# Performance work log

Measured on AMD Instinct MI355X. Metric: run time of the kernel, lower is better.

Reference implementation:

```python
import jax, jax.numpy as jnp
import numpy as np

H = 256
EPS = 1e-5

def setup_inputs() -> dict:
    key = jax.random.key(0)
    ks = jax.random.split(key, 9)
    B, T = 2048, 512
    x = jax.random.randint(ks[0], (B, T, 1), 0, 10).astype(jnp.float32)
    # parameters (torch nn.Linear stores weight as [out,in]; we store [in,out])
    W_embed = jax.random.normal(ks[1], (1, H), jnp.float32) * 0.5
    b_embed = jax.random.normal(ks[2], (H,), jnp.float32) * 0.05
    W_update = jax.random.normal(ks[3], (H, H), jnp.float32) * (1.0 / np.sqrt(H))
    b_update = jax.random.normal(ks[4], (H,), jnp.float32) * 0.05
    gamma = jnp.ones((H,), jnp.float32)
    beta = jnp.zeros((H,), jnp.float32)
    W_out = jax.random.normal(ks[5], (H, 10), jnp.float32) * (1.0 / np.sqrt(H))
    b_out = jax.random.normal(ks[6], (10,), jnp.float32) * 0.05
    return {"x": x, "W_embed": W_embed, "b_embed": b_embed,
            "W_update": W_update, "b_update": b_update,
            "gamma": gamma, "beta": beta, "W_out": W_out, "b_out": b_out}

def _layernorm(h, gamma, beta):
    mu = jnp.mean(h, axis=-1, keepdims=True)
    var = jnp.mean(jnp.square(h - mu), axis=-1, keepdims=True)
    return (h - mu) * jax.lax.rsqrt(var + EPS) * gamma + beta

def reference(x, W_embed, b_embed, W_update, b_update, gamma, beta, W_out, b_out):
    B, T, _ = x.shape
    xt = jnp.transpose(x, (1, 0, 2))  # [T, B, 1]

    def step(h, x_t):
        inp = jnp.tanh(x_t @ W_embed + b_embed)           # [B, H]
        h = jnp.tanh((inp + h) @ W_update + b_update)     # [B, H]
        h = _layernorm(h, gamma, beta)
        return h, None

    h0 = jnp.zeros((B, H), x.dtype)
    h_final, _ = jax.lax.scan(step, h0, xt)
    return h_final @ W_out + b_out                        # [B, 10]
```

## Files before the change

### kernel.cpp

```cpp
#include <hip/hip_runtime.h>
#include <hip/hip_fp16.h>
#include <cstdint>

#define T_STEPS 512
#define HDIM    256
#define ROWS    8
#define LN_EPS  1e-5f

typedef _Float16 half8   __attribute__((ext_vector_type(8)));
typedef _Float16 half4v  __attribute__((ext_vector_type(4)));
typedef float    float4v __attribute__((ext_vector_type(4)));
typedef float    float2v __attribute__((ext_vector_type(2)));
typedef int      int4v   __attribute__((ext_vector_type(4)));
typedef int      int2v   __attribute__((ext_vector_type(2)));

#if __has_builtin(__builtin_amdgcn_permlane32_swap)
#define HAS_PL32 1
#else
#define HAS_PL32 0
#endif
#if __has_builtin(__builtin_amdgcn_permlane16_swap)
#define HAS_PL16 1
#else
#define HAS_PL16 0
#endif

struct __align__(16) Smem {
  _Float16 Bp[2][4096];
  float    gb[10][268];
  float    wg[260];
  float    wb[260];
  float    red[2][8][20];
  int      xi[8][516];
};

__device__ __forceinline__ float tanh_fast(float x) {
  float e = __expf(2.0f * x);
  float r = __builtin_amdgcn_rcpf(e + 1.0f);
  return fmaf(-2.0f, r, 1.0f);
}
__device__ __forceinline__ float dpp_ror8(float v) {
  return __int_as_float(__builtin_amdgcn_mov_dpp(__float_as_int(v), 0x128, 0xf, 0xf, true));
}
__device__ __forceinline__ float swz_xor16(float v) {
  return __int_as_float(__builtin_amdgcn_ds_swizzle(__float_as_int(v), 0x401F));
}
__device__ __forceinline__ float sum_xor16(float v) {
#if HAS_PL16
  int2v r2 = __builtin_amdgcn_permlane16_swap(__float_as_int(v), __float_as_int(v), false, false);
  return __int_as_float(r2[0]) + __int_as_float(r2[1]);
#else
  return v + swz_xor16(v);
#endif
}
__device__ __forceinline__ float sum_xor32(float v) {
#if HAS_PL32
  int2v r2 = __builtin_amdgcn_permlane32_swap(__float_as_int(v), __float_as_int(v), false, false);
  return __int_as_float(r2[0]) + __int_as_float(r2[1]);
#else
  return v + __shfl_xor(v, 32, 64);
#endif
}

__global__ __launch_bounds__(512, 1)
void rnn_scan_kernel(const float* __restrict__ x,
                     const float* __restrict__ we,  const float* __restrict__ be,
                     const float* __restrict__ Wu,  const float* __restrict__ bu,
                     const float* __restrict__ gma, const float* __restrict__ bta,
                     const float* __restrict__ Wo,  const float* __restrict__ bo,
                     float* __restrict__ out)
{
  __shared__ Smem sm;
  const int tid = threadIdx.x;
  const int wv  = tid >> 6;
  const int l   = tid & 63;
  const int q   = l >> 4;
  const int m   = l & 15;
  const int sel = m >> 3;
  const int r   = m & 7;
  const int r0  = blockIdx.x * ROWS;

  for (int i = tid; i < ROWS * T_STEPS; i += 512) {
    const int rr = i >> 9, c = i & (T_STEPS - 1);
    int xv = (int)x[(size_t)(r0 + rr) * T_STEPS + c];
    xv = xv < 0 ? 0 : (xv > 9 ? 9 : xv);
    sm.xi[rr][c] = xv;
  }
  if (tid < ROWS) {
    sm.xi[tid][512] = 0; sm.xi[tid][513] = 0;
    sm.xi[tid][514] = 0; sm.xi[tid][515] = 0;
  }

  float* et = reinterpret_cast<float*>(&sm.Bp[0][0]);
  if (tid < HDIM) {
    const float wek = we[tid], bek = be[tid];
    #pragma unroll
    for (int v = 0; v < 10; ++v)
      et[v*HDIM + tid] = tanh_fast(fmaf((float)v, wek, bek));
  }
  __syncthreads();

  {
    const int g = tid >> 8;
    const int n = tid & 255;
    float acc[5] = {0,0,0,0,0};
    float accx = 0.0f;
    const int vb = g * 5;
    for (int k = 0; k < HDIM; ++k) {
      const float wk = Wu[(size_t)k*HDIM + n];
      #pragma unroll
      for (int v = 0; v < 5; ++v) acc[v] = fmaf(et[(vb+v)*HDIM + k], wk, acc[v]);
      const float xk = g ? bta[k] : gma[k];
      accx = fmaf(xk, wk, accx);
    }
    const float bun = bu[n];
    #pragma unroll
    for (int v = 0; v < 5; ++v) sm.gb[vb+v][n] = acc[v] + bun;
    if (g == 0) sm.wg[n] = accx; else sm.wb[n] = accx;
  }
  __syncthreads();

  if (tid < HDIM) {
    const float wbn = sm.wb[tid];
    #pragma unroll
    for (int v = 0; v < 10; ++v) sm.gb[v][tid] += wbn;
  }
  {
    uint32_t* p = reinterpret_cast<uint32_t*>(&sm.Bp[0][0]);
    for (int i = tid; i < 4096; i += 512) p[i] = 0u;
  }
  if (tid < 320) (&sm.red[0][0][0])[tid] = 0.0f;

  half8 Whi[2][8], Wlo[2][8];
  #pragma unroll
  for (int nt = 0; nt < 2; ++nt) {
    const int n = wv*32 + nt*16 + m;
    #pragma unroll
    for (int kt = 0; kt < 8; ++kt) {
      const int k0 = kt*32 + q*8;
      half8 hi, lo;
      #pragma unroll
      for (int j = 0; j < 8; ++j) {
        float v = Wu[(size_t)(k0 + j)*HDIM + n];
        _Float16 h = (_Float16)v;
        hi[j] = h;
        lo[j] = (_Float16)((v - (float)h) * 2048.0f);
      }
      Whi[nt][kt] = hi; Wlo[nt][kt] = lo;
    }
  }
  const int n_sel = wv*32 + sel*16 + q*4;
  const float4v gmr = *reinterpret_cast<const float4v*>(&gma[n_sel]);
  __syncthreads();
  const float4v wgr = *reinterpret_cast<const float4v*>(&sm.wg[n_sel]);

  const float c1 = 4.8828125e-4f;
  const float* gbp = &sm.gb[0][n_sel];
  float4v th4;

  const int rdoff = l * 8;
  const int woff  = wv*512 + (2*sel + (q>>1))*128 + r*8 + (q&1)*4;

  int4v xQ = *reinterpret_cast<const int4v*>(&sm.xi[r][0]);
  float4v gbv_n = *reinterpret_cast<const float4v*>(gbp + xQ[0]*268);

  for (int k = 0; k < T_STEPS/4; ++k) {
    const int4v xQn = *reinterpret_cast<const int4v*>(&sm.xi[r][k*4 + 4]);
    #pragma unroll
    for (int e = 0; e < 4; ++e) {
      const int rb = e & 1, wb = rb ^ 1;

      const float4v pq = *reinterpret_cast<const float4v*>(&sm.red[rb][r][q*4]);

      const float4v gbv = gbv_n;
      const int xv2 = (e < 3) ? xQ[e + 1] : xQn[0];

      const _Float16* pbB = &sm.Bp[rb][rdoff];
      float4v d10, d11, d20, d21;
      d10 = 0.0f; d11 = 0.0f; d20 = 0.0f; d21 = 0.0f;
      #pragma unroll
      for (int kt = 0; kt < 8; ++kt) {
        const half8 b = *reinterpret_cast<const half8*>(pbB + kt*512);
        d10 = __builtin_amdgcn_mfma_f32_16x16x32_f16(Whi[0][kt], b, d10, 0, 0, 0);
        d11 = __builtin_amdgcn_mfma_f32_16x16x32_f16(Whi[1][kt], b, d11, 0, 0, 0);
        d20 = __builtin_amdgcn_mfma_f32_16x16x32_f16(Wlo[0][kt], b, d20, 0, 0, 0);
        d21 = __builtin_amdgcn_mfma_f32_16x16x32_f16(Wlo[1][kt], b, d21, 0, 0, 0);
      }

      gbv_n = *reinterpret_cast<const float4v*>(gbp + xv2*268);

      float S  = pq[0] + pq[2];
      float Sq = pq[1] + pq[3];
      S  = sum_xor32(sum_xor16(S));
      Sq = sum_xor32(sum_xor16(Sq));
      const float mu  = S * (1.0f/256.0f);
      const float var = fmaf(Sq, 1.0f/256.0f, -mu*mu);
      const float rs  = __builtin_amdgcn_rsqf(var + LN_EPS);
      const float nrsmu = -rs * mu;
      const float rsc   = rs * c1;

      const float csA = sel ? rsc : rs;
      float4v sendv, locv;
      #pragma unroll
      for (int i2 = 0; i2 < 4; ++i2) {
        const float pA = sel ? d10[i2] : d11[i2];
        const float pB = sel ? 0.0f    : d21[i2];
        sendv[i2] = fmaf(csA, pA, rsc * pB);
        const float qA = sel ? d11[i2] : d10[i2];
        const float qB = sel ? 0.0f    : d20[i2];
        locv[i2]  = fmaf(csA, qA, rsc * qB);
      }
      float4v recv;
      #pragma unroll
      for (int i2 = 0; i2 < 4; ++i2) recv[i2] = dpp_ror8(sendv[i2]);

      float s = 0.0f, sq = 0.0f;
      half4v hi4, lo4;
      #pragma unroll
      for (int i2 = 0; i2 < 4; ++i2) {
        const float base = fmaf(nrsmu, wgr[i2], gbv[i2]);
        const float pre  = locv[i2] + recv[i2] + base;
        const float th   = tanh_fast(pre);
        th4[i2] = th; s += th; sq = fmaf(th, th, sq);
        const float g2 = th * gmr[i2];
        const _Float16 h16 = (_Float16)g2;
        hi4[i2] = h16;
        lo4[i2] = (_Float16)((g2 - (float)h16) * 2048.0f);
      }
      s  += dpp_ror8(s);  s  = sum_xor32(sum_xor16(s));
      sq += dpp_ror8(sq); sq = sum_xor32(sum_xor16(sq));

      _Float16* wp = &sm.Bp[wb][woff];
      *reinterpret_cast<half4v*>(wp)      = hi4;
      *reinterpret_cast<half4v*>(wp + 64) = lo4;
      if (l < 8) {
        float2v v2; v2[0] = s; v2[1] = sq;
        *reinterpret_cast<float2v*>(&sm.red[wb][l][wv*2]) = v2;
      }
      __syncthreads();
    }
    xQ = xQn;
  }

  float mu, rs;
  {
    const float4v pq = *reinterpret_cast<const float4v*>(&sm.red[0][r][q*4]);
    float S  = pq[0] + pq[2];
    float Sq = pq[1] + pq[3];
    S  = sum_xor32(sum_xor16(S));
    Sq = sum_xor32(sum_xor16(Sq));
    mu = S * (1.0f/256.0f);
    const float var = fmaf(Sq, 1.0f/256.0f, -mu*mu);
    rs = __builtin_amdgcn_rsqf(var + LN_EPS);
  }
  float* hf = reinterpret_cast<float*>(&sm.gb[0][0]);
  {
    const float4v btv = *reinterpret_cast<const float4v*>(&bta[n_sel]);
    float4v h4;
    #pragma unroll
    for (int e = 0; e < 4; ++e)
      h4[e] = fmaf((th4[e] - mu) * rs, gmr[e], btv[e]);
    *reinterpret_cast<float4v*>(&hf[r*260 + n_sel]) = h4;
  }
  __syncthreads();
  if (tid < ROWS*10) {
    const int rr = tid / 10, o = tid % 10;
    float acc = bo[o];
    #pragma unroll 4
    for (int n = 0; n < HDIM; ++n)
      acc = fmaf(hf[rr*260 + n], Wo[n*10 + o], acc);
    out[(size_t)(r0 + rr)*10 + o] = acc;
  }
}

extern "C" void kernel_launch(void* const* d_in, const int* in_sizes, int n_in,
                              void* d_out, int out_size, void* d_ws, size_t ws_size,
                              hipStream_t stream) {
  const float* x  = (const float*)d_in[0];
  const float* we = (const float*)d_in[1];
  const float* be = (const float*)d_in[2];
  const float* Wu = (const float*)d_in[3];
  const float* bu = (const float*)d_in[4];
  const float* ga = (const float*)d_in[5];
  const float* bt = (const float*)d_in[6];
  const float* Wo = (const float*)d_in[7];
  const float* bo = (const float*)d_in[8];
  const int B = in_sizes[0] / T_STEPS;
  dim3 grid(B / ROWS), block(512);
  rnn_scan_kernel<<<grid, block, 0, stream>>>(x, we, be, Wu, bu, ga, bt, Wo, bo,
                                              (float*)d_out);
}
```

Baseline: 606.8 us.

## Split hidden dimension across 16 waves instead of 8 per block

New measurement: 725.1 us. +19.5%, slower.

```diff
diff --git a/kernel.cpp b/kernel.cpp
--- a/kernel.cpp
+++ b/kernel.cpp
@@ -8,7 +8,7 @@
 #define LN_EPS  1e-5f
 
 typedef _Float16 half8   __attribute__((ext_vector_type(8)));
-typedef _Float16 half4v  __attribute__((ext_vector_type(4)));
+typedef _Float16 half2v  __attribute__((ext_vector_type(2)));
 typedef float    float4v __attribute__((ext_vector_type(4)));
 typedef float    float2v __attribute__((ext_vector_type(2)));
 typedef int      int4v   __attribute__((ext_vector_type(4)));
@@ -30,7 +30,7 @@
   float    gb[10][268];
   float    wg[260];
   float    wb[260];
-  float    red[2][8][20];
+  float    red[2][8][40];
   int      xi[8][516];
 };
 
@@ -62,7 +62,7 @@
 #endif
 }
 
-__global__ __launch_bounds__(512, 1)
+__global__ __launch_bounds__(1024, 1)
 void rnn_scan_kernel(const float* __restrict__ x,
                      const float* __restrict__ we,  const float* __restrict__ be,
                      const float* __restrict__ Wu,  const float* __restrict__ bu,
@@ -80,7 +80,7 @@
   const int r   = m & 7;
   const int r0  = blockIdx.x * ROWS;
 
-  for (int i = tid; i < ROWS * T_STEPS; i += 512) {
+  for (int i = tid; i < ROWS * T_STEPS; i += 1024) {
     const int rr = i >> 9, c = i & (T_STEPS - 1);
     int xv = (int)x[(size_t)(r0 + rr) * T_STEPS + c];
     xv = xv < 0 ? 0 : (xv > 9 ? 9 : xv);
@@ -100,7 +100,7 @@
   }
   __syncthreads();
 
-  {
+  if (tid < 512) {
     const int g = tid >> 8;
     const int n = tid & 255;
     float acc[5] = {0,0,0,0,0};
@@ -127,14 +127,13 @@
   }
   {
     uint32_t* p = reinterpret_cast<uint32_t*>(&sm.Bp[0][0]);
-    for (int i = tid; i < 4096; i += 512) p[i] = 0u;
-  }
-  if (tid < 320) (&sm.red[0][0][0])[tid] = 0.0f;
-
-  half8 Whi[2][8], Wlo[2][8];
-  #pragma unroll
-  for (int nt = 0; nt < 2; ++nt) {
-    const int n = wv*32 + nt*16 + m;
+    for (int i = tid; i < 4096; i += 1024) p[i] = 0u;
+  }
+  if (tid < 640) (&sm.red[0][0][0])[tid] = 0.0f;
+
+  half8 Whi[8], Wlo[8];
+  {
+    const int n = wv*16 + m;
     #pragma unroll
     for (int kt = 0; kt < 8; ++kt) {
       const int k0 = kt*32 + q*8;
@@ -146,23 +145,23 @@
         hi[j] = h;
         lo[j] = (_Float16)((v - (float)h) * 2048.0f);
       }
-      Whi[nt][kt] = hi; Wlo[nt][kt] = lo;
+      Whi[kt] = hi; Wlo[kt] = lo;
     }
   }
-  const int n_sel = wv*32 + sel*16 + q*4;
-  const float4v gmr = *reinterpret_cast<const float4v*>(&gma[n_sel]);
-  __syncthreads();
-  const float4v wgr = *reinterpret_cast<const float4v*>(&sm.wg[n_sel]);
+  const int n2 = wv*16 + q*4 + sel*2;
+  const float2v gmr = *reinterpret_cast<const float2v*>(&gma[n2]);
+  __syncthreads();
+  const float2v wgr = *reinterpret_cast<const float2v*>(&sm.wg[n2]);
 
   const float c1 = 4.8828125e-4f;
-  const float* gbp = &sm.gb[0][n_sel];
-  float4v th4;
+  const float* gbp = &sm.gb[0][n2];
+  float2v th2;
 
   const int rdoff = l * 8;
-  const int woff  = wv*512 + (2*sel + (q>>1))*128 + r*8 + (q&1)*4;
+  const int woff  = (n2 >> 5)*512 + ((n2 >> 3) & 3)*128 + r*8 + (n2 & 7);
 
   int4v xQ = *reinterpret_cast<const int4v*>(&sm.xi[r][0]);
-  float4v gbv_n = *reinterpret_cast<const float4v*>(gbp + xQ[0]*268);
+  float2v gbv_n = *reinterpret_cast<const float2v*>(gbp + xQ[0]*268);
 
   for (int k = 0; k < T_STEPS/4; ++k) {
     const int4v xQn = *reinterpret_cast<const int4v*>(&sm.xi[r][k*4 + 4]);
@@ -170,69 +169,60 @@
     for (int e = 0; e < 4; ++e) {
       const int rb = e & 1, wb = rb ^ 1;
 
-      const float4v pq = *reinterpret_cast<const float4v*>(&sm.red[rb][r][q*4]);
-
-      const float4v gbv = gbv_n;
+      const float4v pq = *reinterpret_cast<const float4v*>(&sm.red[rb][r][(q*2 + sel)*4]);
+
+      const float2v gbv = gbv_n;
       const int xv2 = (e < 3) ? xQ[e + 1] : xQn[0];
 
       const _Float16* pbB = &sm.Bp[rb][rdoff];
-      float4v d10, d11, d20, d21;
-      d10 = 0.0f; d11 = 0.0f; d20 = 0.0f; d21 = 0.0f;
+      float4v d1, d2;
+      d1 = 0.0f; d2 = 0.0f;
       #pragma unroll
       for (int kt = 0; kt < 8; ++kt) {
         const half8 b = *reinterpret_cast<const half8*>(pbB + kt*512);
-        d10 = __builtin_amdgcn_mfma_f32_16x16x32_f16(Whi[0][kt], b, d10, 0, 0, 0);
-        d11 = __builtin_amdgcn_mfma_f32_16x16x32_f16(Whi[1][kt], b, d11, 0, 0, 0);
-        d20 = __builtin_amdgcn_mfma_f32_16x16x32_f16(Wlo[0][kt], b, d20, 0, 0, 0);
-        d21 = __builtin_amdgcn_mfma_f32_16x16x32_f16(Wlo[1][kt], b, d21, 0, 0, 0);
-      }
-
-      gbv_n = *reinterpret_cast<const float4v*>(gbp + xv2*268);
+        d1 = __builtin_amdgcn_mfma_f32_16x16x32_f16(Whi[kt], b, d1, 0, 0, 0);
+        d2 = __builtin_amdgcn_mfma_f32_16x16x32_f16(Wlo[kt], b, d2, 0, 0, 0);
+      }
+
+      gbv_n = *reinterpret_cast<const float2v*>(gbp + xv2*268);
 
       float S  = pq[0] + pq[2];
       float Sq = pq[1] + pq[3];
-      S  = sum_xor32(sum_xor16(S));
-      Sq = sum_xor32(sum_xor16(Sq));
+      S  += dpp_ror8(S);  S  = sum_xor32(sum_xor16(S));
+      Sq += dpp_ror8(Sq); Sq = sum_xor32(sum_xor16(Sq));
       const float mu  = S * (1.0f/256.0f);
       const float var = fmaf(Sq, 1.0f/256.0f, -mu*mu);
       const float rs  = __builtin_amdgcn_rsqf(var + LN_EPS);
       const float nrsmu = -rs * mu;
       const float rsc   = rs * c1;
 
-      const float csA = sel ? rsc : rs;
-      float4v sendv, locv;
-      #pragma unroll
-      for (int i2 = 0; i2 < 4; ++i2) {
-        const float pA = sel ? d10[i2] : d11[i2];
-        const float pB = sel ? 0.0f    : d21[i2];
-        sendv[i2] = fmaf(csA, pA, rsc * pB);
-        const float qA = sel ? d11[i2] : d10[i2];
-        const float qB = sel ? 0.0f    : d20[i2];
-        locv[i2]  = fmaf(csA, qA, rsc * qB);
-      }
-      float4v recv;
-      #pragma unroll
-      for (int i2 = 0; i2 < 4; ++i2) recv[i2] = dpp_ror8(sendv[i2]);
+      float4v Av, fullv;
+      #pragma unroll
+      for (int i2 = 0; i2 < 4; ++i2)
+        Av[i2] = sel ? rsc * d1[i2] : fmaf(rs, d1[i2], rsc * d2[i2]);
+      #pragma unroll
+      for (int i2 = 0; i2 < 4; ++i2)
+        fullv[i2] = Av[i2] + dpp_ror8(Av[i2]);
 
       float s = 0.0f, sq = 0.0f;
-      half4v hi4, lo4;
-      #pragma unroll
-      for (int i2 = 0; i2 < 4; ++i2) {
-        const float base = fmaf(nrsmu, wgr[i2], gbv[i2]);
-        const float pre  = locv[i2] + recv[i2] + base;
+      half2v hi2, lo2;
+      #pragma unroll
+      for (int j = 0; j < 2; ++j) {
+        const float base = fmaf(nrsmu, wgr[j], gbv[j]);
+        const float pre  = fullv[sel*2 + j] + base;
         const float th   = tanh_fast(pre);
-        th4[i2] = th; s += th; sq = fmaf(th, th, sq);
-        const float g2 = th * gmr[i2];
+        th2[j] = th; s += th; sq = fmaf(th, th, sq);
+        const float g2 = th * gmr[j];
         const _Float16 h16 = (_Float16)g2;
-        hi4[i2] = h16;
-        lo4[i2] = (_Float16)((g2 - (float)h16) * 2048.0f);
+        hi2[j] = h16;
+        lo2[j] = (_Float16)((g2 - (float)h16) * 2048.0f);
       }
       s  += dpp_ror8(s);  s  = sum_xor32(sum_xor16(s));
       sq += dpp_ror8(sq); sq = sum_xor32(sum_xor16(sq));
 
       _Float16* wp = &sm.Bp[wb][woff];
-      *reinterpret_cast<half4v*>(wp)      = hi4;
-      *reinterpret_cast<half4v*>(wp + 64) = lo4;
+      *reinterpret_cast<half2v*>(wp)      = hi2;
+      *reinterpret_cast<half2v*>(wp + 64) = lo2;
       if (l < 8) {
         float2v v2; v2[0] = s; v2[1] = sq;
         *reinterpret_cast<float2v*>(&sm.red[wb][l][wv*2]) = v2;
@@ -244,23 +234,23 @@
 
   float mu, rs;
   {
-    const float4v pq = *reinterpret_cast<const float4v*>(&sm.red[0][r][q*4]);
+    const float4v pq = *reinterpret_cast<const float4v*>(&sm.red[0][r][(q*2 + sel)*4]);
     float S  = pq[0] + pq[2];
     float Sq = pq[1] + pq[3];
-    S  = sum_xor32(sum_xor16(S));
-    Sq = sum_xor32(sum_xor16(Sq));
+    S  += dpp_ror8(S);  S  = sum_xor32(sum_xor16(S));
+    Sq += dpp_ror8(Sq); Sq = sum_xor32(sum_xor16(Sq));
     mu = S * (1.0f/256.0f);
     const float var = fmaf(Sq, 1.0f/256.0f, -mu*mu);
     rs = __builtin_amdgcn_rsqf(var + LN_EPS);
   }
   float* hf = reinterpret_cast<float*>(&sm.gb[0][0]);
   {
-    const float4v btv = *reinterpret_cast<const float4v*>(&bta[n_sel]);
-    float4v h4;
-    #pragma unroll
-    for (int e = 0; e < 4; ++e)
-      h4[e] = fmaf((th4[e] - mu) * rs, gmr[e], btv[e]);
-    *reinterpret_cast<float4v*>(&hf[r*260 + n_sel]) = h4;
+    const float2v btv = *reinterpret_cast<const float2v*>(&bta[n2]);
+    float2v h2;
+    #pragma unroll
+    for (int j = 0; j < 2; ++j)
+      h2[j] = fmaf((th2[j] - mu) * rs, gmr[j], btv[j]);
+    *reinterpret_cast<float2v*>(&hf[r*260 + n2]) = h2;
   }
   __syncthreads();
   if (tid < ROWS*10) {
@@ -286,7 +276,7 @@
   const float* Wo = (const float*)d_in[7];
   const float* bo = (const float*)d_in[8];
   const int B = in_sizes[0] / T_STEPS;
-  dim3 grid(B / ROWS), block(512);
+  dim3 grid(B / ROWS), block(1024);
   rnn_scan_kernel<<<grid, block, 0, stream>>>(x, we, be, Wu, bu, ga, bt, Wo, bo,
                                               (float*)d_out);
 }
```

## Split MFMA chain to overlap LayerNorm stats with matmul, use packed fp16 converts

Applied to the files above, without the earlier changes.

New measurement: 573.0 us, median of 3. 1.06x faster.

```diff
diff --git a/kernel.cpp b/kernel.cpp
--- a/kernel.cpp
+++ b/kernel.cpp
@@ -9,6 +9,7 @@
 
 typedef _Float16 half8   __attribute__((ext_vector_type(8)));
 typedef _Float16 half4v  __attribute__((ext_vector_type(4)));
+typedef __fp16   fp16x2  __attribute__((ext_vector_type(2)));
 typedef float    float4v __attribute__((ext_vector_type(4)));
 typedef float    float2v __attribute__((ext_vector_type(2)));
 typedef int      int4v   __attribute__((ext_vector_type(4)));
@@ -176,19 +177,22 @@
       const int xv2 = (e < 3) ? xQ[e + 1] : xQn[0];
 
       const _Float16* pbB = &sm.Bp[rb][rdoff];
+      half8 bfr[8];
+      #pragma unroll
+      for (int kt = 0; kt < 8; ++kt)
+        bfr[kt] = *reinterpret_cast<const half8*>(pbB + kt*512);
+
       float4v d10, d11, d20, d21;
       d10 = 0.0f; d11 = 0.0f; d20 = 0.0f; d21 = 0.0f;
+      __builtin_amdgcn_s_setprio(1);
       #pragma unroll
       for (int kt = 0; kt < 8; ++kt) {
-        const half8 b = *reinterpret_cast<const half8*>(pbB + kt*512);
-        d10 = __builtin_amdgcn_mfma_f32_16x16x32_f16(Whi[0][kt], b, d10, 0, 0, 0);
-        d11 = __builtin_amdgcn_mfma_f32_16x16x32_f16(Whi[1][kt], b, d11, 0, 0, 0);
-        d20 = __builtin_amdgcn_mfma_f32_16x16x32_f16(Wlo[0][kt], b, d20, 0, 0, 0);
-        d21 = __builtin_amdgcn_mfma_f32_16x16x32_f16(Wlo[1][kt], b, d21, 0, 0, 0);
-      }
+        d10 = __builtin_amdgcn_mfma_f32_16x16x32_f16(Whi[0][kt], bfr[kt], d10, 0, 0, 0);
+        d20 = __builtin_amdgcn_mfma_f32_16x16x32_f16(Wlo[0][kt], bfr[kt], d20, 0, 0, 0);
+      }
+      __builtin_amdgcn_s_setprio(0);
 
       gbv_n = *reinterpret_cast<const float4v*>(gbp + xv2*268);
-
       float S  = pq[0] + pq[2];
       float Sq = pq[1] + pq[3];
       S  = sum_xor32(sum_xor16(S));
@@ -198,8 +202,16 @@
       const float rs  = __builtin_amdgcn_rsqf(var + LN_EPS);
       const float nrsmu = -rs * mu;
       const float rsc   = rs * c1;
-
-      const float csA = sel ? rsc : rs;
+      const float csA   = sel ? rsc : rs;
+
+      __builtin_amdgcn_s_setprio(1);
+      #pragma unroll
+      for (int kt = 0; kt < 8; ++kt) {
+        d11 = __builtin_amdgcn_mfma_f32_16x16x32_f16(Whi[1][kt], bfr[kt], d11, 0, 0, 0);
+        d21 = __builtin_amdgcn_mfma_f32_16x16x32_f16(Wlo[1][kt], bfr[kt], d21, 0, 0, 0);
+      }
+      __builtin_amdgcn_s_setprio(0);
+
       float4v sendv, locv;
       #pragma unroll
       for (int i2 = 0; i2 < 4; ++i2) {
@@ -215,18 +227,29 @@
       for (int i2 = 0; i2 < 4; ++i2) recv[i2] = dpp_ror8(sendv[i2]);
 
       float s = 0.0f, sq = 0.0f;
-      half4v hi4, lo4;
+      float g2v[4];
       #pragma unroll
       for (int i2 = 0; i2 < 4; ++i2) {
         const float base = fmaf(nrsmu, wgr[i2], gbv[i2]);
         const float pre  = locv[i2] + recv[i2] + base;
         const float th   = tanh_fast(pre);
         th4[i2] = th; s += th; sq = fmaf(th, th, sq);
-        const float g2 = th * gmr[i2];
-        const _Float16 h16 = (_Float16)g2;
-        hi4[i2] = h16;
-        lo4[i2] = (_Float16)((g2 - (float)h16) * 2048.0f);
-      }
+        g2v[i2] = th * gmr[i2];
+      }
+      const fp16x2 h01 = __builtin_amdgcn_cvt_pkrtz(g2v[0], g2v[1]);
+      const fp16x2 h23 = __builtin_amdgcn_cvt_pkrtz(g2v[2], g2v[3]);
+      const float r0f = (g2v[0] - (float)h01[0]) * 2048.0f;
+      const float r1f = (g2v[1] - (float)h01[1]) * 2048.0f;
+      const float r2f = (g2v[2] - (float)h23[0]) * 2048.0f;
+      const float r3f = (g2v[3] - (float)h23[1]) * 2048.0f;
+      const fp16x2 l01 = __builtin_amdgcn_cvt_pkrtz(r0f, r1f);
+      const fp16x2 l23 = __builtin_amdgcn_cvt_pkrtz(r2f, r3f);
+      half4v hi4, lo4;
+      hi4[0] = (_Float16)h01[0]; hi4[1] = (_Float16)h01[1];
+      hi4[2] = (_Float16)h23[0]; hi4[3] = (_Float16)h23[1];
+      lo4[0] = (_Float16)l01[0]; lo4[1] = (_Float16)l01[1];
+      lo4[2] = (_Float16)l23[0]; lo4[3] = (_Float16)l23[1];
+
       s  += dpp_ror8(s);  s  = sum_xor32(sum_xor16(s));
       sq += dpp_ror8(sq); sq = sum_xor32(sum_xor16(sq));
 
```
